# Kernel optimization log

Measured on AMD Instinct MI355X. Metric: run time of the kernel, lower is better.

The kernel has to match this reference:

```python
import math
import jax, jax.numpy as jnp
import numpy as np

L, H, D, FF, V, S = 12, 12, 768, 3072, 32000, 1024
HD = D // H
EPS = 1e-5
B, T = 2, 1024


def layernorm(x, w, b):
    mu = jnp.mean(x, axis=-1, keepdims=True)
    var = jnp.mean(jnp.square(x - mu), axis=-1, keepdims=True)
    return (x - mu) * jax.lax.rsqrt(var + EPS) * w + b


def setup_inputs() -> dict:
    key = jax.random.key(0)
    ks = jax.random.split(key, 12)
    std = 0.02
    std_res = 0.02 / math.sqrt(2 * L)  # out_proj / down_proj scaled init
    return {
        "input_ids": jax.random.randint(ks[0], (B, T), 0, V),
        "tok_emb": jax.random.normal(ks[1], (V, D), jnp.float32) * std,
        "pos_emb": jax.random.normal(ks[2], (S, D), jnp.float32) * std,
        "ln1_w": jnp.ones((L, D), jnp.float32),
        "ln1_b": jnp.zeros((L, D), jnp.float32),
        "qkv_w": jax.random.normal(ks[3], (L, 3 * D, D), jnp.float32) * std,
        "out_w": jax.random.normal(ks[4], (L, D, D), jnp.float32) * std_res,
        "ln2_w": jnp.ones((L, D), jnp.float32),
        "ln2_b": jnp.zeros((L, D), jnp.float32),
        "up_w": jax.random.normal(ks[5], (L, FF, D), jnp.float32) * std,
        "down_w": jax.random.normal(ks[6], (L, D, FF), jnp.float32) * std_res,
        "lnf_w": jnp.ones((D,), jnp.float32),
        "lnf_b": jnp.zeros((D,), jnp.float32),
    }


def reference(input_ids, tok_emb, pos_emb, ln1_w, ln1_b, qkv_w, out_w,
              ln2_w, ln2_b, up_w, down_w, lnf_w, lnf_b):
    b, t = input_ids.shape
    x = tok_emb[input_ids] + pos_emb[:t]  # (B,T,D); dropout = eval no-op
    causal = jnp.tril(jnp.ones((t, t), bool))  # (T,T)
    scale = 1.0 / math.sqrt(HD)

    def block(x, p):
        l1w, l1b, qkvw, ow, l2w, l2b, uw, dw = p
        h = layernorm(x, l1w, l1b)
        qkv = h @ qkvw.T  # (B,T,3D)
        q, k, v = jnp.split(qkv, 3, axis=-1)
        q = q.reshape(b, t, H, HD)
        k = k.reshape(b, t, H, HD)
        v = v.reshape(b, t, H, HD)
        scores = jnp.einsum('bihd,bjhd->bhij', q, k) * scale
        scores = jnp.where(causal, scores, -jnp.inf)
        probs = jax.nn.softmax(scores, axis=-1)  # attn_dropout = eval no-op
        o = jnp.einsum('bhij,bjhd->bihd', probs, v).reshape(b, t, D)
        x = x + o @ ow.T
        h2 = layernorm(x, l2w, l2b)
        x = x + jax.nn.gelu(h2 @ uw.T, approximate=False) @ dw.T
        return x, None

    x, _ = jax.lax.scan(block, x, (ln1_w, ln1_b, qkv_w, out_w, ln2_w, ln2_b, up_w, down_w))
    x = layernorm(x, lnf_w, lnf_b)
    logits = x @ tok_emb.T  # tied lm_head
    return logits
```

## Files before the change

### kernel.cpp

```cpp
#include <hip/hip_runtime.h>
#include <hip/hip_bf16.h>
#include <math.h>

#define L_  12
#define H_  12
#define D_  768
#define FF_ 3072
#define V_  32000
#define T_  1024
#define B_  2
#define BT_ (B_*T_)

typedef unsigned short ushort_t;
typedef unsigned int   uint_t;
typedef __bf16 bf16x8 __attribute__((ext_vector_type(8)));
typedef float  f32x4  __attribute__((ext_vector_type(4)));

__device__ __forceinline__ uint_t f2bf1(float f) {
    uint_t u = __builtin_bit_cast(uint_t, f);
    return (u + 0x7FFFu + ((u >> 16) & 1u)) >> 16;
}
__device__ __forceinline__ uint_t f2bf2(float lo, float hi) {
    return f2bf1(lo) | (f2bf1(hi) << 16);
}
__device__ __forceinline__ float bf2f(ushort_t u) {
    return __builtin_bit_cast(float, (uint_t)u << 16);
}

__device__ __forceinline__ void gl_lds16(const ushort_t* g, ushort_t* l) {
    __builtin_amdgcn_global_load_lds(
        (const __attribute__((address_space(1))) uint_t*)g,
        (__attribute__((address_space(3))) uint_t*)l, 16, 0, 0);
}

__global__ __launch_bounds__(256) void cast_bf16(const float* __restrict__ in,
                                                 ushort_t* __restrict__ out, int n8)
{
    for (int i = blockIdx.x * 256 + threadIdx.x; i < n8; i += gridDim.x * 256) {
        const float4* p = (const float4*)(in + (size_t)i * 8);
        float4 a = p[0], b = p[1];
        *(uint4*)(out + (size_t)i * 8) =
            make_uint4(f2bf2(a.x,a.y), f2bf2(a.z,a.w), f2bf2(b.x,b.y), f2bf2(b.z,b.w));
    }
}

__global__ __launch_bounds__(256) void cast_layer(const float* __restrict__ q,
    const float* __restrict__ o, const float* __restrict__ u, const float* __restrict__ d,
    ushort_t* __restrict__ out)
{
    const int N0 = 3*D_*D_/8, N1 = N0 + D_*D_/8, N2 = N1 + FF_*D_/8, N3 = N2 + D_*FF_/8;
    for (int i = blockIdx.x * 256 + threadIdx.x; i < N3; i += gridDim.x * 256) {
        const float* src;
        if      (i < N0) src = q + (size_t)i * 8;
        else if (i < N1) src = o + (size_t)(i - N0) * 8;
        else if (i < N2) src = u + (size_t)(i - N1) * 8;
        else             src = d + (size_t)(i - N2) * 8;
        const float4* p = (const float4*)src;
        float4 a = p[0], b = p[1];
        *(uint4*)(out + (size_t)i * 8) =
            make_uint4(f2bf2(a.x,a.y), f2bf2(a.z,a.w), f2bf2(b.x,b.y), f2bf2(b.z,b.w));
    }
}

#define EPI_F32   0
#define EPI_BF16  1
#define EPI_GELU  2
#define EPI_PART  3
#define EPI_QKV   4

template <int EPI, int BM, int KS>
__global__ __launch_bounds__(256) void gemm_bt(
    const ushort_t* __restrict__ A, const ushort_t* __restrict__ W,
    const float* R, void* Cv, ushort_t* __restrict__ Vt, int N, int K, int Kc)
{
    constexpr int MI = BM / 32;
    constexpr int AH = BM * 32;
    constexpr int BH = 128 * 32;
    __shared__ ushort_t As[2 * AH];
    __shared__ ushort_t Bs[2 * BH];

    const int tid  = threadIdx.x;
    const int w    = tid >> 6;
    const int lane = tid & 63;

    const int nwg = gridDim.x;
    int swz = (blockIdx.x & 7) * (nwg >> 3) + (blockIdx.x >> 3);
    constexpr int MT = 2048 / BM;
    const int mt = swz & (MT - 1);
    int rest     = swz / MT;
    const int ks = rest & (KS - 1);
    const int nt = rest / KS;
    const int m0 = mt * BM, n0 = nt * 128;
    const int kb = ks * Kc;

    const int srow = lane >> 2;
    const int scol = ((lane & 3) ^ ((srow >> 1) & 3)) * 8;
    const ushort_t* gA = A + (size_t)(m0 + w * (BM / 4) + srow) * K + scol;
    const ushort_t* gW = W + (size_t)(n0 + w * 32 + srow) * K + scol;
    const size_t row16 = (size_t)16 * K;

    const int lr = lane & 15;
    const int lg = lane >> 4;
    const int wm = (w >> 1) * (BM / 2);
    const int wn = (w & 1) * 64;

    f32x4 acc[MI][4] = {};

    auto stage = [&](int buf, int k0) {
        ushort_t* lA = As + buf * AH + w * (BM / 4) * 32;
        ushort_t* lB = Bs + buf * BH + w * 1024;
        #pragma unroll
        for (int i = 0; i < BM / 64; ++i)
            gl_lds16(gA + k0 + i * row16, lA + i * 512);
        #pragma unroll
        for (int i = 0; i < 2; ++i)
            gl_lds16(gW + k0 + i * row16, lB + i * 512);
    };

    stage(0, kb);
    __syncthreads();
    int cur = 0;
    for (int k0 = kb; k0 < kb + Kc; k0 += 32) {
        if (k0 + 32 < kb + Kc) stage(cur ^ 1, k0 + 32);
        const ushort_t* Ab = As + cur * AH;
        const ushort_t* Bb = Bs + cur * BH;
        __builtin_amdgcn_s_setprio(1);
        {
            bf16x8 av[MI], bv[4];
            #pragma unroll
            for (int i = 0; i < MI; ++i) {
                int rr = wm + i * 16 + lr;
                int ch = lg ^ ((rr >> 1) & 3);
                av[i] = *(const bf16x8*)&Ab[rr * 32 + ch * 8];
            }
            #pragma unroll
            for (int j = 0; j < 4; ++j) {
                int rr = wn + j * 16 + lr;
                int ch = lg ^ ((rr >> 1) & 3);
                bv[j] = *(const bf16x8*)&Bb[rr * 32 + ch * 8];
            }
            #pragma unroll
            for (int i = 0; i < MI; ++i)
                #pragma unroll
                for (int j = 0; j < 4; ++j)
                    acc[i][j] = __builtin_amdgcn_mfma_f32_16x16x32_bf16(av[i], bv[j], acc[i][j], 0, 0, 0);
        }
        __builtin_amdgcn_s_setprio(0);
        __syncthreads();
        cur ^= 1;
    }

    float*    Cf = (float*)Cv;
    ushort_t* Cb = (ushort_t*)Cv;
    ushort_t* Pp = (EPI == EPI_PART) ? ((ushort_t*)Cv + (size_t)ks * BT_ * D_) : nullptr;
    const int rbase = lg * 4;
    #pragma unroll
    for (int i = 0; i < MI; ++i) {
        #pragma unroll
        for (int j = 0; j < 4; ++j) {
            const int row0 = m0 + wm + i * 16 + rbase;
            const int col  = n0 + wn + j * 16 + lr;
            if (EPI == EPI_QKV) {
                if (col < 1536) {
                    #pragma unroll
                    for (int r = 0; r < 4; ++r)
                        Cb[(size_t)(row0 + r) * 2304 + col] = (ushort_t)f2bf1(acc[i][j][r]);
                } else {
                    const int hh = (col - 1536) >> 6, dd = (col - 1536) & 63;
                    const int bb = row0 >> 10,        tt = row0 & 1023;
                    uint2 pk;
                    pk.x = f2bf2(acc[i][j][0], acc[i][j][1]);
                    pk.y = f2bf2(acc[i][j][2], acc[i][j][3]);
                    *(uint2*)&Vt[(((size_t)bb * H_ + hh) * 64 + dd) * T_ + tt] = pk;
                }
            } else {
                #pragma unroll
                for (int r = 0; r < 4; ++r) {
                    size_t idx = (size_t)(row0 + r) * N + col;
                    float v = acc[i][j][r];
                    if (EPI == EPI_F32)  Cf[idx] = v;
                    if (EPI == EPI_BF16) Cb[idx] = (ushort_t)f2bf1(v);
                    if (EPI == EPI_GELU) Cb[idx] = (ushort_t)f2bf1(0.5f * v * (1.0f + erff(v * 0.70710678118654752f)));
                    if (EPI == EPI_PART) Pp[idx] = (ushort_t)f2bf1(v);
                }
            }
        }
    }
}

__global__ __launch_bounds__(512, 2) void gemm256(
    const ushort_t* __restrict__ A, const ushort_t* __restrict__ W,
    float* __restrict__ C, int N, int K)
{
    __shared__ ushort_t Ls[2][2][256 * 64];

    const int tid  = threadIdx.x;
    const int w    = tid >> 6;
    const int lane = tid & 63;

    const int nwg = gridDim.x;
    int swz = (blockIdx.x & 7) * (nwg >> 3) + (blockIdx.x >> 3);
    const int mt = swz & 7;
    const int nt = swz >> 3;
    const int m0 = mt * 256, n0 = nt * 256;

    const int trow = tid >> 3;
    const int tchk = (tid & 7) ^ (trow & 7);
    const ushort_t* gA = A + (size_t)(m0 + trow) * K + tchk * 8;
    const ushort_t* gW = W + (size_t)(n0 + trow) * K + tchk * 8;

    const int lr = lane & 15;
    const int lg = lane >> 4;
    const int wm = (w >> 2) * 128;
    const int wn = (w & 3) * 64;

    f32x4 acc[8][4] = {};

    auto stage = [&](int buf, int k0) {
        #pragma unroll
        for (int seg = 0; seg < 4; ++seg) {
            gl_lds16(gA + (size_t)(seg * 64) * K + k0, &Ls[buf][0][seg * 4096 + w * 512]);
            gl_lds16(gW + (size_t)(seg * 64) * K + k0, &Ls[buf][1][seg * 4096 + w * 512]);
        }
    };

    stage(0, 0);
    __syncthreads();
    int cur = 0;
    const int NT = K / 64;
    for (int t = 0; t < NT; ++t) {
        if (t + 1 < NT) stage(cur ^ 1, (t + 1) * 64);
        const ushort_t* Ab = Ls[cur][0];
        const ushort_t* Bb = Ls[cur][1];
        bf16x8 bv[4][2];
        #pragma unroll
        for (int nf = 0; nf < 4; ++nf) {
            int rr = wn + nf * 16 + lr;
            #pragma unroll
            for (int kk = 0; kk < 2; ++kk) {
                int ch = (kk * 4 + lg) ^ (rr & 7);
                bv[nf][kk] = *(const bf16x8*)&Bb[rr * 64 + ch * 8];
            }
        }
        __builtin_amdgcn_s_setprio(1);
        #pragma unroll
        for (int mf = 0; mf < 8; ++mf) {
            int rr = wm + mf * 16 + lr;
            int ch0 = lg ^ (rr & 7);
            int ch1 = (4 + lg) ^ (rr & 7);
            bf16x8 a0 = *(const bf16x8*)&Ab[rr * 64 + ch0 * 8];
            bf16x8 a1 = *(const bf16x8*)&Ab[rr * 64 + ch1 * 8];
            #pragma unroll
            for (int nf = 0; nf < 4; ++nf) {
                acc[mf][nf] = __builtin_amdgcn_mfma_f32_16x16x32_bf16(a0, bv[nf][0], acc[mf][nf], 0, 0, 0);
                acc[mf][nf] = __builtin_amdgcn_mfma_f32_16x16x32_bf16(a1, bv[nf][1], acc[mf][nf], 0, 0, 0);
            }
        }
        __builtin_amdgcn_s_setprio(0);
        __syncthreads();
        cur ^= 1;
    }

    const int rbase = lg * 4;
    #pragma unroll
    for (int mf = 0; mf < 8; ++mf) {
        #pragma unroll
        for (int nf = 0; nf < 4; ++nf) {
            #pragma unroll
            for (int r = 0; r < 4; ++r) {
                int row = m0 + wm + mf * 16 + rbase + r;
                int col = n0 + wn + nf * 16 + lr;
                C[(size_t)row * N + col] = acc[mf][nf][r];
            }
        }
    }
}

__global__ __launch_bounds__(64) void attn_mfma(const ushort_t* __restrict__ qkv,
    const ushort_t* __restrict__ vt, ushort_t* __restrict__ o)
{
    __shared__ ushort_t Ps[16 * 136];

    int swz = (blockIdx.x & 7) * 192 + (blockIdx.x >> 3);
    const int bh  = swz >> 6;
    const int qtl = 63 - (swz & 63);
    const int b   = bh / H_;
    const int h   = bh % H_;
    const int lane = threadIdx.x;
    const int l15  = lane & 15;
    const int lg   = lane >> 4;
    const int qbase = qtl * 16;
    const int qlast = qbase + 15;

    const ushort_t* qp = qkv + ((size_t)(b * T_) + qbase + l15) * 2304 + h * 64 + lg * 8;
    bf16x8 qf0 = *(const bf16x8*)qp;
    bf16x8 qf1 = *(const bf16x8*)(qp + 32);

    f32x4 od[4] = {};
    float mr[4] = {-INFINITY, -INFINITY, -INFINITY, -INFINITY};
    float lr[4] = {0.f, 0.f, 0.f, 0.f};

    const ushort_t* kbase = qkv + (size_t)(b * T_) * 2304 + 768 + h * 64;
    const ushort_t* vbase = vt + (size_t)bh * 64 * T_;
    const float SC = 0.18033688011112042f;

    for (int j0 = 0; j0 <= qlast; j0 += 128) {
        f32x4 s[8];
        __builtin_amdgcn_s_setprio(1);
        #pragma unroll
        for (int n = 0; n < 8; ++n) {
            if (j0 + 16 * n <= qlast) {
                const ushort_t* kr = kbase + (size_t)(j0 + 16 * n + l15) * 2304 + lg * 8;
                bf16x8 kf0 = *(const bf16x8*)kr;
                bf16x8 kf1 = *(const bf16x8*)(kr + 32);
                f32x4 a = {};
                a = __builtin_amdgcn_mfma_f32_16x16x32_bf16(qf0, kf0, a, 0, 0, 0);
                a = __builtin_amdgcn_mfma_f32_16x16x32_bf16(qf1, kf1, a, 0, 0, 0);
                s[n] = a;
            } else {
                s[n] = f32x4{-INFINITY, -INFINITY, -INFINITY, -INFINITY};
            }
        }
        __builtin_amdgcn_s_setprio(0);

        #pragma unroll
        for (int n = 0; n < 8; ++n) {
            #pragma unroll
            for (int r = 0; r < 4; ++r) {
                float v = s[n][r] * SC;
                int jg = j0 + 16 * n + l15;
                int qg = qbase + lg * 4 + r;
                if (jg > qg) v = -INFINITY;
                s[n][r] = v;
            }
        }

        float al[4];
        #pragma unroll
        for (int r = 0; r < 4; ++r) {
            float tm = fmaxf(fmaxf(fmaxf(s[0][r], s[1][r]), fmaxf(s[2][r], s[3][r])),
                             fmaxf(fmaxf(s[4][r], s[5][r]), fmaxf(s[6][r], s[7][r])));
            tm = fmaxf(tm, __shfl_xor(tm, 1, 64));
            tm = fmaxf(tm, __shfl_xor(tm, 2, 64));
            tm = fmaxf(tm, __shfl_xor(tm, 4, 64));
            tm = fmaxf(tm, __shfl_xor(tm, 8, 64));
            float mn = fmaxf(mr[r], tm);
            al[r] = exp2f(mr[r] - mn);
            mr[r] = mn;
        }
        #pragma unroll
        for (int n = 0; n < 8; ++n)
            #pragma unroll
            for (int r = 0; r < 4; ++r)
                s[n][r] = exp2f(s[n][r] - mr[r]);
        #pragma unroll
        for (int r = 0; r < 4; ++r) {
            float ps = (s[0][r] + s[1][r]) + (s[2][r] + s[3][r]);
            ps += (s[4][r] + s[5][r]) + (s[6][r] + s[7][r]);
            ps += __shfl_xor(ps, 1, 64);
            ps += __shfl_xor(ps, 2, 64);
            ps += __shfl_xor(ps, 4, 64);
            ps += __shfl_xor(ps, 8, 64);
            lr[r] = lr[r] * al[r] + ps;
        }
        #pragma unroll
        for (int n = 0; n < 4; ++n)
            #pragma unroll
            for (int r = 0; r < 4; ++r)
                od[n][r] *= al[r];

        #pragma unroll
        for (int n = 0; n < 8; ++n)
            #pragma unroll
            for (int r = 0; r < 4; ++r)
                Ps[(lg * 4 + r) * 136 + 16 * n + l15] = (ushort_t)f2bf1(s[n][r]);

        __builtin_amdgcn_s_setprio(1);
        #pragma unroll
        for (int kc = 0; kc < 4; ++kc) {
            if (j0 + kc * 32 <= qlast) {
                bf16x8 pa = *(const bf16x8*)&Ps[l15 * 136 + kc * 32 + lg * 8];
                #pragma unroll
                for (int nn = 0; nn < 4; ++nn) {
                    bf16x8 vf = *(const bf16x8*)&vbase[(size_t)(16 * nn + l15) * T_ + j0 + kc * 32 + lg * 8];
                    od[nn] = __builtin_amdgcn_mfma_f32_16x16x32_bf16(pa, vf, od[nn], 0, 0, 0);
                }
            }
        }
        __builtin_amdgcn_s_setprio(0);
    }

    #pragma unroll
    for (int r = 0; r < 4; ++r) {
        float inv = 1.0f / lr[r];
        int row = qbase + lg * 4 + r;
        ushort_t* op = o + ((size_t)(b * T_ + row)) * 768 + h * 64 + l15;
        #pragma unroll
        for (int nn = 0; nn < 4; ++nn)
            op[16 * nn] = (ushort_t)f2bf1(od[nn][r] * inv);
    }
}

__device__ __forceinline__ void ln_body(float v0, float v1, float v2,
    const float* __restrict__ w, const float* __restrict__ bia,
    ushort_t* __restrict__ orow, int tid)
{
    float s  = v0 + v1 + v2;
    float s2 = v0 * v0 + v1 * v1 + v2 * v2;
    #pragma unroll
    for (int off = 32; off > 0; off >>= 1) {
        s  += __shfl_down(s,  off, 64);
        s2 += __shfl_down(s2, off, 64);
    }
    __shared__ float sh[8];
    const int wave = tid >> 6;
    if ((tid & 63) == 0) { sh[wave] = s; sh[4 + wave] = s2; }
    __syncthreads();
    float S  = sh[0] + sh[1] + sh[2] + sh[3];
    float S2 = sh[4] + sh[5] + sh[6] + sh[7];
    float mean = S * (1.f / 768.f);
    float var  = S2 * (1.f / 768.f) - mean * mean;
    float inv  = rsqrtf(var + 1e-5f);
    orow[tid]       = (ushort_t)f2bf1((v0 - mean) * inv * w[tid]       + bia[tid]);
    orow[tid + 256] = (ushort_t)f2bf1((v1 - mean) * inv * w[tid + 256] + bia[tid + 256]);
    orow[tid + 512] = (ushort_t)f2bf1((v2 - mean) * inv * w[tid + 512] + bia[tid + 512]);
}

__global__ __launch_bounds__(256) void ln_red4(float* __restrict__ x,
    const ushort_t* __restrict__ P, const float* __restrict__ w,
    const float* __restrict__ bia, ushort_t* __restrict__ out)
{
    const int row = blockIdx.x;
    const int tid = threadIdx.x;
    const size_t base = (size_t)row * 768;
    const size_t st = (size_t)BT_ * D_;
    float v0 = x[base + tid];
    float v1 = x[base + tid + 256];
    float v2 = x[base + tid + 512];
    #pragma unroll
    for (int p = 0; p < 4; ++p) {
        v0 += bf2f(P[p * st + base + tid]);
        v1 += bf2f(P[p * st + base + tid + 256]);
        v2 += bf2f(P[p * st + base + tid + 512]);
    }
    x[base + tid]       = v0;
    x[base + tid + 256] = v1;
    x[base + tid + 512] = v2;
    ln_body(v0, v1, v2, w, bia, out + base, tid);
}

__global__ __launch_bounds__(256) void embed_ln(const int* __restrict__ ids,
    const float* __restrict__ tok, const float* __restrict__ pos,
    const float* __restrict__ w, const float* __restrict__ bia,
    float* __restrict__ x, ushort_t* __restrict__ out)
{
    const int bt = blockIdx.x;
    const int t  = bt % T_;
    const int id = ids[bt];
    const int tid = threadIdx.x;
    const float* tr = tok + (size_t)id * 768;
    const float* pr = pos + (size_t)t * 768;
    const size_t base = (size_t)bt * 768;
    float v0 = tr[tid]       + pr[tid];
    float v1 = tr[tid + 256] + pr[tid + 256];
    float v2 = tr[tid + 512] + pr[tid + 512];
    x[base + tid]       = v0;
    x[base + tid + 256] = v1;
    x[base + tid + 512] = v2;
    ln_body(v0, v1, v2, w, bia, out + base, tid);
}

extern "C" void kernel_launch(void* const* d_in, const int* in_sizes, int n_in,
                              void* d_out, int out_size, void* d_ws, size_t ws_size,
                              hipStream_t stream)
{
    const int*   ids   = (const int*)  d_in[0];
    const float* tok   = (const float*)d_in[1];
    const float* pos   = (const float*)d_in[2];
    const float* ln1w  = (const float*)d_in[3];
    const float* ln1b  = (const float*)d_in[4];
    const float* qkvw  = (const float*)d_in[5];
    const float* outw  = (const float*)d_in[6];
    const float* ln2w  = (const float*)d_in[7];
    const float* ln2b  = (const float*)d_in[8];
    const float* upw   = (const float*)d_in[9];
    const float* downw = (const float*)d_in[10];
    const float* lnfw  = (const float*)d_in[11];
    const float* lnfb  = (const float*)d_in[12];
    float* out = (float*)d_out;

    char* ws = (char*)d_ws;
    ushort_t* h    = (ushort_t*)ws;
    float*    x    = (float*)   (ws + 3145728);
    ushort_t* qkv  = (ushort_t*)(ws + 9437184);
    ushort_t* o    = qkv  + (size_t)BT_ * 3 * D_;
    ushort_t* vt   = o    + (size_t)BT_ * D_;
    ushort_t* ffh  = vt   + (size_t)B_ * H_ * 64 * T_;
    ushort_t* P4   = (ushort_t*)(ws + 37748736);
    ushort_t* layerW = (ushort_t*)(ws + 50331648);
    ushort_t* tokW   = (ushort_t*)(ws + 67108864);

    ushort_t* qkvwB  = layerW;
    ushort_t* outwB  = qkvwB + (size_t)3 * D_ * D_;
    ushort_t* upwB   = outwB + (size_t)D_ * D_;
    ushort_t* downwB = upwB  + (size_t)FF_ * D_;

    for (int l = 0; l < L_; ++l) {
        cast_layer<<<1024, 256, 0, stream>>>(
            qkvw  + (size_t)l * 3 * D_ * D_,
            outw  + (size_t)l * D_ * D_,
            upw   + (size_t)l * FF_ * D_,
            downw + (size_t)l * D_ * FF_, layerW);

        if (l == 0)
            embed_ln<<<BT_, 256, 0, stream>>>(ids, tok, pos, ln1w, ln1b, x, h);
        else
            ln_red4<<<BT_, 256, 0, stream>>>(x, P4, ln1w + l * D_, ln1b + l * D_, h);

        gemm_bt<EPI_QKV, 64, 1><<<32 * (3 * D_ / 128), 256, 0, stream>>>(
            h, qkvwB, nullptr, qkv, vt, 3 * D_, D_, D_);

        attn_mfma<<<B_ * H_ * (T_ / 16), 64, 0, stream>>>(qkv, vt, o);

        gemm_bt<EPI_PART, 64, 4><<<32 * (D_ / 128) * 4, 256, 0, stream>>>(
            o, outwB, nullptr, P4, nullptr, D_, D_, D_ / 4);

        ln_red4<<<BT_, 256, 0, stream>>>(x, P4, ln2w + l * D_, ln2b + l * D_, h);

        gemm_bt<EPI_GELU, 64, 1><<<32 * (FF_ / 128), 256, 0, stream>>>(
            h, upwB, nullptr, ffh, nullptr, FF_, D_, D_);

        gemm_bt<EPI_PART, 64, 4><<<32 * (D_ / 128) * 4, 256, 0, stream>>>(
            ffh, downwB, nullptr, P4, nullptr, D_, FF_, FF_ / 4);
    }

    ln_red4<<<BT_, 256, 0, stream>>>(x, P4, lnfw, lnfb, h);

    cast_bf16<<<2048, 256, 0, stream>>>(tok, tokW, V_ * D_ / 8);
    gemm256<<<(2048 / 256) * (V_ / 256), 512, 0, stream>>>(h, tokW, out, V_, D_);
}
```

Before: 1.929 ms.

## Double GEMM K-tile to 64 and fuse weight cast into LayerNorm launch

The bf16 GEMM now stages 64-wide K slices per buffer instead of 32, with a new 8-chunk XOR swizzle, and runs two MFMA sub-steps per iteration. This halves the number of barrier and stage iterations at the cost of twice the LDS per block, which may reduce occupancy. Separately, the per-layer fp32-to-bf16 weight cast is merged into the LayerNorm/embedding kernel as extra blocks, removing one launch per layer and letting the cast overlap with the LayerNorm work. The unused residual pointer argument is dropped.

```diff
diff --git a/kernel.cpp b/kernel.cpp
--- a/kernel.cpp
+++ b/kernel.cpp
@@ -44,12 +44,12 @@
     }
 }
 
-__global__ __launch_bounds__(256) void cast_layer(const float* __restrict__ q,
+__device__ __forceinline__ void cast_body(const float* __restrict__ q,
     const float* __restrict__ o, const float* __restrict__ u, const float* __restrict__ d,
-    ushort_t* __restrict__ out)
+    ushort_t* __restrict__ out, int bid, int nb)
 {
     const int N0 = 3*D_*D_/8, N1 = N0 + D_*D_/8, N2 = N1 + FF_*D_/8, N3 = N2 + D_*FF_/8;
-    for (int i = blockIdx.x * 256 + threadIdx.x; i < N3; i += gridDim.x * 256) {
+    for (int i = bid * 256 + threadIdx.x; i < N3; i += nb * 256) {
         const float* src;
         if      (i < N0) src = q + (size_t)i * 8;
         else if (i < N1) src = o + (size_t)(i - N0) * 8;
@@ -71,11 +71,11 @@
 template <int EPI, int BM, int KS>
 __global__ __launch_bounds__(256) void gemm_bt(
     const ushort_t* __restrict__ A, const ushort_t* __restrict__ W,
-    const float* R, void* Cv, ushort_t* __restrict__ Vt, int N, int K, int Kc)
+    void* Cv, ushort_t* __restrict__ Vt, int N, int K, int Kc)
 {
     constexpr int MI = BM / 32;
-    constexpr int AH = BM * 32;
-    constexpr int BH = 128 * 32;
+    constexpr int AH = BM * 64;
+    constexpr int BH = 128 * 64;
     __shared__ ushort_t As[2 * AH];
     __shared__ ushort_t Bs[2 * BH];
 
@@ -93,11 +93,11 @@
     const int m0 = mt * BM, n0 = nt * 128;
     const int kb = ks * Kc;
 
-    const int srow = lane >> 2;
-    const int scol = ((lane & 3) ^ ((srow >> 1) & 3)) * 8;
+    const int srow = lane >> 3;
+    const int scol = ((lane & 7) ^ srow) * 8;
     const ushort_t* gA = A + (size_t)(m0 + w * (BM / 4) + srow) * K + scol;
     const ushort_t* gW = W + (size_t)(n0 + w * 32 + srow) * K + scol;
-    const size_t row16 = (size_t)16 * K;
+    const size_t row8 = (size_t)8 * K;
 
     const int lr = lane & 15;
     const int lg = lane >> 4;
@@ -107,37 +107,38 @@
     f32x4 acc[MI][4] = {};
 
     auto stage = [&](int buf, int k0) {
-        ushort_t* lA = As + buf * AH + w * (BM / 4) * 32;
-        ushort_t* lB = Bs + buf * BH + w * 1024;
-        #pragma unroll
-        for (int i = 0; i < BM / 64; ++i)
-            gl_lds16(gA + k0 + i * row16, lA + i * 512);
-        #pragma unroll
-        for (int i = 0; i < 2; ++i)
-            gl_lds16(gW + k0 + i * row16, lB + i * 512);
+        ushort_t* lA = As + buf * AH + w * (BM / 4) * 64;
+        ushort_t* lB = Bs + buf * BH + w * 2048;
+        #pragma unroll
+        for (int i = 0; i < BM / 32; ++i)
+            gl_lds16(gA + k0 + i * row8, lA + i * 512);
+        #pragma unroll
+        for (int i = 0; i < 4; ++i)
+            gl_lds16(gW + k0 + i * row8, lB + i * 512);
     };
 
     stage(0, kb);
     __syncthreads();
     int cur = 0;
-    for (int k0 = kb; k0 < kb + Kc; k0 += 32) {
-        if (k0 + 32 < kb + Kc) stage(cur ^ 1, k0 + 32);
+    for (int k0 = kb; k0 < kb + Kc; k0 += 64) {
+        if (k0 + 64 < kb + Kc) stage(cur ^ 1, k0 + 64);
         const ushort_t* Ab = As + cur * AH;
         const ushort_t* Bb = Bs + cur * BH;
         __builtin_amdgcn_s_setprio(1);
-        {
+        #pragma unroll
+        for (int kk = 0; kk < 2; ++kk) {
             bf16x8 av[MI], bv[4];
             #pragma unroll
             for (int i = 0; i < MI; ++i) {
                 int rr = wm + i * 16 + lr;
-                int ch = lg ^ ((rr >> 1) & 3);
-                av[i] = *(const bf16x8*)&Ab[rr * 32 + ch * 8];
+                int ch = (lg + 4 * kk) ^ (rr & 7);
+                av[i] = *(const bf16x8*)&Ab[rr * 64 + ch * 8];
             }
             #pragma unroll
             for (int j = 0; j < 4; ++j) {
                 int rr = wn + j * 16 + lr;
-                int ch = lg ^ ((rr >> 1) & 3);
-                bv[j] = *(const bf16x8*)&Bb[rr * 32 + ch * 8];
+                int ch = (lg + 4 * kk) ^ (rr & 7);
+                bv[j] = *(const bf16x8*)&Bb[rr * 64 + ch * 8];
             }
             #pragma unroll
             for (int i = 0; i < MI; ++i)
@@ -426,11 +427,10 @@
     orow[tid + 512] = (ushort_t)f2bf1((v2 - mean) * inv * w[tid + 512] + bia[tid + 512]);
 }
 
-__global__ __launch_bounds__(256) void ln_red4(float* __restrict__ x,
+__device__ __forceinline__ void ln_red4_body(float* __restrict__ x,
     const ushort_t* __restrict__ P, const float* __restrict__ w,
-    const float* __restrict__ bia, ushort_t* __restrict__ out)
-{
-    const int row = blockIdx.x;
+    const float* __restrict__ bia, ushort_t* __restrict__ out, int row)
+{
     const int tid = threadIdx.x;
     const size_t base = (size_t)row * 768;
     const size_t st = (size_t)BT_ * D_;
@@ -449,25 +449,52 @@
     ln_body(v0, v1, v2, w, bia, out + base, tid);
 }
 
-__global__ __launch_bounds__(256) void embed_ln(const int* __restrict__ ids,
+__global__ __launch_bounds__(256) void ln_red4_cast(float* __restrict__ x,
+    const ushort_t* __restrict__ P, const float* __restrict__ w,
+    const float* __restrict__ bia, ushort_t* __restrict__ out,
+    const float* __restrict__ cq, const float* __restrict__ co,
+    const float* __restrict__ cu, const float* __restrict__ cd,
+    ushort_t* __restrict__ wout)
+{
+    if (blockIdx.x < 2048)
+        ln_red4_body(x, P, w, bia, out, blockIdx.x);
+    else
+        cast_body(cq, co, cu, cd, wout, blockIdx.x - 2048, 1024);
+}
+
+__global__ __launch_bounds__(256) void ln_red4(float* __restrict__ x,
+    const ushort_t* __restrict__ P, const float* __restrict__ w,
+    const float* __restrict__ bia, ushort_t* __restrict__ out)
+{
+    ln_red4_body(x, P, w, bia, out, blockIdx.x);
+}
+
+__global__ __launch_bounds__(256) void embed_ln_cast(const int* __restrict__ ids,
     const float* __restrict__ tok, const float* __restrict__ pos,
     const float* __restrict__ w, const float* __restrict__ bia,
-    float* __restrict__ x, ushort_t* __restrict__ out)
-{
-    const int bt = blockIdx.x;
-    const int t  = bt % T_;
-    const int id = ids[bt];
-    const int tid = threadIdx.x;
-    const float* tr = tok + (size_t)id * 768;
-    const float* pr = pos + (size_t)t * 768;
-    const size_t base = (size_t)bt * 768;
-    float v0 = tr[tid]       + pr[tid];
-    float v1 = tr[tid + 256] + pr[tid + 256];
-    float v2 = tr[tid + 512] + pr[tid + 512];
-    x[base + tid]       = v0;
-    x[base + tid + 256] = v1;
-    x[base + tid + 512] = v2;
-    ln_body(v0, v1, v2, w, bia, out + base, tid);
+    float* __restrict__ x, ushort_t* __restrict__ out,
+    const float* __restrict__ cq, const float* __restrict__ co,
+    const float* __restrict__ cu, const float* __restrict__ cd,
+    ushort_t* __restrict__ wout)
+{
+    if (blockIdx.x < 2048) {
+        const int bt = blockIdx.x;
+        const int t  = bt % T_;
+        const int id = ids[bt];
+        const int tid = threadIdx.x;
+        const float* tr = tok + (size_t)id * 768;
+        const float* pr = pos + (size_t)t * 768;
+        const size_t base = (size_t)bt * 768;
+        float v0 = tr[tid]       + pr[tid];
+        float v1 = tr[tid + 256] + pr[tid + 256];
+        float v2 = tr[tid + 512] + pr[tid + 512];
+        x[base + tid]       = v0;
+        x[base + tid + 256] = v1;
+        x[base + tid + 512] = v2;
+        ln_body(v0, v1, v2, w, bia, out + base, tid);
+    } else {
+        cast_body(cq, co, cu, cd, wout, blockIdx.x - 2048, 1024);
+    }
 }
 
 extern "C" void kernel_launch(void* const* d_in, const int* in_sizes, int n_in,
@@ -506,32 +533,33 @@
     ushort_t* downwB = upwB  + (size_t)FF_ * D_;
 
     for (int l = 0; l < L_; ++l) {
-        cast_layer<<<1024, 256, 0, stream>>>(
-            qkvw  + (size_t)l * 3 * D_ * D_,
-            outw  + (size_t)l * D_ * D_,
-            upw   + (size_t)l * FF_ * D_,
-            downw + (size_t)l * D_ * FF_, layerW);
+        const float* cq = qkvw  + (size_t)l * 3 * D_ * D_;
+        const float* co = outw  + (size_t)l * D_ * D_;
+        const float* cu = upw   + (size_t)l * FF_ * D_;
+        const float* cd = downw + (size_t)l * D_ * FF_;
 
         if (l == 0)
-            embed_ln<<<BT_, 256, 0, stream>>>(ids, tok, pos, ln1w, ln1b, x, h);
+            embed_ln_cast<<<3072, 256, 0, stream>>>(ids, tok, pos, ln1w, ln1b, x, h,
+                                                    cq, co, cu, cd, layerW);
         else
-            ln_red4<<<BT_, 256, 0, stream>>>(x, P4, ln1w + l * D_, ln1b + l * D_, h);
+            ln_red4_cast<<<3072, 256, 0, stream>>>(x, P4, ln1w + l * D_, ln1b + l * D_, h,
+                                                   cq, co, cu, cd, layerW);
 
         gemm_bt<EPI_QKV, 64, 1><<<32 * (3 * D_ / 128), 256, 0, stream>>>(
-            h, qkvwB, nullptr, qkv, vt, 3 * D_, D_, D_);
+            h, qkvwB, qkv, vt, 3 * D_, D_, D_);
 
         attn_mfma<<<B_ * H_ * (T_ / 16), 64, 0, stream>>>(qkv, vt, o);
 
         gemm_bt<EPI_PART, 64, 4><<<32 * (D_ / 128) * 4, 256, 0, stream>>>(
-            o, outwB, nullptr, P4, nullptr, D_, D_, D_ / 4);
+            o, outwB, P4, nullptr, D_, D_, D_ / 4);
 
         ln_red4<<<BT_, 256, 0, stream>>>(x, P4, ln2w + l * D_, ln2b + l * D_, h);
 
         gemm_bt<EPI_GELU, 64, 1><<<32 * (FF_ / 128), 256, 0, stream>>>(
-            h, upwB, nullptr, ffh, nullptr, FF_, D_, D_);
+            h, upwB, ffh, nullptr, FF_, D_, D_);
 
         gemm_bt<EPI_PART, 64, 4><<<32 * (D_ / 128) * 4, 256, 0, stream>>>(
-            ffh, downwB, nullptr, P4, nullptr, D_, FF_, FF_ / 4);
+            ffh, downwB, P4, nullptr, D_, FF_, FF_ / 4);
     }
 
     ln_red4<<<BT_, 256, 0, stream>>>(x, P4, lnfw, lnfb, h);
```

After: 1.821 ms. -5.6%, faster.
